# Kernel optimization log

Hardware: AMD Instinct MI355X
Metric: run time of the kernel (lower is better)

The kernel has to match this reference:

```python
import jax, jax.numpy as jnp
import numpy as np


def setup_inputs() -> dict:
    key = jax.random.key(0)
    x = jax.random.normal(key, (128, 256, 32, 32), dtype=jnp.float32)
    return {"x": x, "iter_num": 5}


def reference(x, iter_num):
    # x: (B, C, H, W)
    B, C, H, W = x.shape
    N = H * W
    xr = x.reshape(B, C, N)
    # Covariance pooling: X @ I_hat @ X^T == (1/N) * Xc @ Xc^T  (I_hat = I/N - J/N^2)
    xc = xr - xr.mean(axis=2, keepdims=True)
    cov = jnp.einsum('bcn,bdn->bcd', xc, xc) / N  # (B, C, C)

    # Newton-Schulz iterative matrix square root
    I = jnp.eye(C, dtype=x.dtype)
    I3 = 3.0 * I
    trace = jnp.trace(cov, axis1=1, axis2=2)[:, None, None]  # norm_A = tr(cov)
    A = cov / trace
    ZY = 0.5 * (I3 - A)
    Y = A @ ZY
    Z = ZY
    for _ in range(1, iter_num - 1):
        ZY = 0.5 * (I3 - Z @ Y)
        Y = Y @ ZY
        Z = ZY @ Z
    YZY = 0.5 * (Y @ (I3 - Z @ Y))
    sqrtm = YZY * jnp.sqrt(trace)  # (B, C, C)

    # Upper-triangular vectorization (row-major, including diagonal)
    r, c = np.triu_indices(C)
    idx = jnp.asarray(r * C + c)
    return sqrtm.reshape(B, C * C)[:, idx]  # (B, C*(C+1)//2)
```

## Files before the change

kernel.cpp:

```cpp
#include <hip/hip_runtime.h>
#include <hip/hip_fp16.h>


typedef _Float16 half8 __attribute__((ext_vector_type(8)));
typedef _Float16 half4 __attribute__((ext_vector_type(4)));
typedef float f32x4 __attribute__((ext_vector_type(4)));

#define OUTPB 32896

__device__ __forceinline__ void gl_lds16(const void* g, void* l) {
  __builtin_amdgcn_global_load_lds(
      (const __attribute__((address_space(1))) void*)g,
      (__attribute__((address_space(3))) void*)l, 16, 0, 0);
}

#define VMB(N) asm volatile("s_waitcnt vmcnt(" #N ")\n\ts_barrier" ::: "memory")
#define LKB()  asm volatile("s_waitcnt lgkmcnt(0)\n\ts_barrier" ::: "memory")

__device__ __forceinline__ void tile_pq(int t, int& p, int& q) {
  p = (t > 3) + (t > 6) + (t > 8);
  int base = p * 4 - (p * (p - 1)) / 2;
  q = p + (t - base);
}

__device__ __forceinline__ void mfma_buf(const _Float16* lA, const _Float16* lB,
                                         f32x4 (&acc)[2][2], int wr, int wc,
                                         int lr, int lk) {
#pragma unroll
  for (int ks = 0; ks < 4; ++ks) {
    half8 af[2], bf[2];
#pragma unroll
    for (int m = 0; m < 2; ++m) {
      int row = wr * 32 + m * 16 + lr;
      int c = (ks * 4 + lk) ^ (row & 7);
      af[m] = *(const half8*)&lA[row * 128 + c * 8];
    }
#pragma unroll
    for (int n = 0; n < 2; ++n) {
      int row = wc * 32 + n * 16 + lr;
      int c = (ks * 4 + lk) ^ (row & 7);
      bf[n] = *(const half8*)&lB[row * 128 + c * 8];
    }
    __builtin_amdgcn_s_setprio(1);
#pragma unroll
    for (int m = 0; m < 2; ++m)
#pragma unroll
      for (int n = 0; n < 2; ++n)
        acc[m][n] = __builtin_amdgcn_mfma_f32_16x16x32_f16(af[m], bf[n], acc[m][n], 0, 0, 0);
    __builtin_amdgcn_s_setprio(0);
  }
}

template <typename F>
__device__ __forceinline__ void store_sym(F f, _Float16* D, size_t boff, int p, int q,
    bool mirror, _Float16* ldsT, f32x4 (&acc)[2][2],
    int wr, int wc, int lr, int lk, int tid) {
#pragma unroll
  for (int m = 0; m < 2; ++m)
#pragma unroll
    for (int n = 0; n < 2; ++n) {
      int il0 = wr * 32 + m * 16 + lk * 4;
      int jl = wc * 32 + n * 16 + lr;
      half4 v4;
#pragma unroll
      for (int r = 0; r < 4; ++r) {
        _Float16 v = f(acc[m][n][r], p * 64 + il0 + r, q * 64 + jl);
        v4[r] = v;
        if (mirror) ldsT[(il0 + r) * 64 + (jl ^ (((il0 + r) & 7) << 3))] = v;
      }
      *(half4*)&D[boff + (size_t)(q * 64 + jl) * 256 + p * 64 + il0] = v4;
    }
  if (mirror) {
    __syncthreads();
#pragma unroll
    for (int pp = 0; pp < 2; ++pp) {
      int u = pp * 256 + tid;
      int im = u >> 3, cu = u & 7;
      half8 v8 = *(const half8*)&ldsT[im * 64 + ((cu ^ (im & 7)) << 3)];
      *(half8*)&D[boff + (size_t)(p * 64 + im) * 256 + q * 64 + cu * 8] = v8;
    }
  }
}

__global__ __launch_bounds__(256, 2) void k_cov(const float* __restrict__ x,
                                                _Float16* __restrict__ covh,
                                                float* __restrict__ trPart) {
  __shared__ _Float16 lds[32768];
  __shared__ float smA[64], smB[64], sred[4];

  const int lin = blockIdx.x + 10 * blockIdx.y;
  const int cid = (lin & 7) * 160 + (lin >> 3);
  const int b = cid / 10, t = cid - 10 * b;
  int p, q; tile_pq(t, p, q);
  const bool diag = (p == q);
  const int tid = threadIdx.x, w = tid >> 6, lane = tid & 63;
  const int wr = w >> 1, wc = w & 1, lr = lane & 15, lk = lane >> 4;

  const float* Ab = x + ((size_t)b * 256 + p * 64) * 1024;
  const float* Bb = x + ((size_t)b * 256 + q * 64) * 1024;

  float4 la[4][2], lb[4][2];
  float rsA[4] = {0.f, 0.f, 0.f, 0.f}, rsB[4] = {0.f, 0.f, 0.f, 0.f};
  f32x4 acc[2][2] = {};

  auto LOAD = [&](int kk) {
#pragma unroll
    for (int it = 0; it < 4; ++it) {
      int row = it * 16 + (tid >> 4);
      int kc = (tid & 15) ^ (row & 7);
      const float4* pa = (const float4*)(Ab + (size_t)row * 1024 + kk * 128 + kc * 8);
      la[it][0] = pa[0]; la[it][1] = pa[1];
      if (!diag) {
        const float4* pb = (const float4*)(Bb + (size_t)row * 1024 + kk * 128 + kc * 8);
        lb[it][0] = pb[0]; lb[it][1] = pb[1];
      }
    }
  };
  auto WRITE = [&](int buf) {
#pragma unroll
    for (int it = 0; it < 4; ++it) {
      int slot = it * 256 + tid;
      float4 a0 = la[it][0], a1 = la[it][1];
      rsA[it] += a0.x + a0.y + a0.z + a0.w + a1.x + a1.y + a1.z + a1.w;
      half8 h;
      h[0] = (_Float16)a0.x; h[1] = (_Float16)a0.y; h[2] = (_Float16)a0.z; h[3] = (_Float16)a0.w;
      h[4] = (_Float16)a1.x; h[5] = (_Float16)a1.y; h[6] = (_Float16)a1.z; h[7] = (_Float16)a1.w;
      *(half8*)&lds[buf * 8192 + slot * 8] = h;
      if (!diag) {
        float4 b0 = lb[it][0], b1 = lb[it][1];
        rsB[it] += b0.x + b0.y + b0.z + b0.w + b1.x + b1.y + b1.z + b1.w;
        half8 g;
        g[0] = (_Float16)b0.x; g[1] = (_Float16)b0.y; g[2] = (_Float16)b0.z; g[3] = (_Float16)b0.w;
        g[4] = (_Float16)b1.x; g[5] = (_Float16)b1.y; g[6] = (_Float16)b1.z; g[7] = (_Float16)b1.w;
        *(half8*)&lds[16384 + buf * 8192 + slot * 8] = g;
      }
    }
  };

  LOAD(0); WRITE(0); LOAD(1);
  __syncthreads();
#pragma unroll 1
  for (int kk = 0; kk < 8; ++kk) {
    int cur = kk & 1;
    mfma_buf(&lds[cur * 8192], diag ? &lds[cur * 8192] : &lds[16384 + cur * 8192],
             acc, wr, wc, lr, lk);
    if (kk < 7) {
      WRITE(cur ^ 1);
      if (kk < 6) LOAD(kk + 2);
    }
    __syncthreads();
  }

#pragma unroll
  for (int it = 0; it < 4; ++it) {
    int row = it * 16 + (tid >> 4);
    float sA = rsA[it];
    sA += __shfl_xor(sA, 1); sA += __shfl_xor(sA, 2);
    sA += __shfl_xor(sA, 4); sA += __shfl_xor(sA, 8);
    if ((lane & 15) == 0) smA[row] = sA * (1.f / 1024.f);
    if (!diag) {
      float sB = rsB[it];
      sB += __shfl_xor(sB, 1); sB += __shfl_xor(sB, 2);
      sB += __shfl_xor(sB, 4); sB += __shfl_xor(sB, 8);
      if ((lane & 15) == 0) smB[row] = sB * (1.f / 1024.f);
    }
  }
  __syncthreads();

  if (diag) {
    float tp = 0.f;
#pragma unroll
    for (int m = 0; m < 2; ++m)
#pragma unroll
      for (int n = 0; n < 2; ++n)
#pragma unroll
        for (int r = 0; r < 4; ++r) {
          int il = wr * 32 + m * 16 + lk * 4 + r, jl = wc * 32 + n * 16 + lr;
          if (il == jl) tp += acc[m][n][r] * (1.f / 1024.f) - smA[il] * smA[il];
        }
#pragma unroll
    for (int o = 32; o; o >>= 1) tp += __shfl_down(tp, o);
    if (lane == 0) sred[w] = tp;
    __syncthreads();
    if (tid == 0) trPart[b * 4 + p] = sred[0] + sred[1] + sred[2] + sred[3];
  }

  const float* smBp = diag ? smA : smB;
  store_sym([&](float a, int i, int j) {
              return (_Float16)(a * (1.f / 1024.f) - smA[i & 63] * smBp[j & 63]);
            }, covh, (size_t)b * 65536, p, q, !diag, lds, acc, wr, wc, lr, lk, tid);
}

enum { EPI_S2 = 0, EPI_ZY = 1, EPI_YZ = 2, EPI_OUT = 3 };

struct GP {
  const _Float16 *A0, *B0, *A1, *B1;
  _Float16 *D0, *D1;
  const _Float16* covh;
  const float* trP;
  float* outF;
};

template <int EPI>
__global__ __launch_bounds__(256, 2) void k_gemm(GP g) {
  __shared__ _Float16 lds[32768];

  const int lin = blockIdx.x + 10 * blockIdx.y;
  const int cid = (lin & 7) * 160 + (lin >> 3);
  const int b = cid / 10, t = cid - 10 * b;
  int p, q; tile_pq(t, p, q);
  const bool diag = (p == q);
  const bool share = diag && (EPI == EPI_S2);
  const int tid = threadIdx.x, w = tid >> 6, lane = tid & 63;
  const int wr = w >> 1, wc = w & 1, lr = lane & 15, lk = lane >> 4;

  const _Float16* Ag = g.A0;
  const _Float16* Bg = g.B0;
  _Float16* Dg = g.D0;
  if constexpr (EPI == EPI_YZ) {
    if (blockIdx.z) { Ag = g.A1; Bg = g.B1; Dg = g.D1; }
  }
  const size_t boff = (size_t)b * 65536;
  const _Float16* Ap = Ag + boff + (size_t)p * 64 * 256;
  const _Float16* Bp = Bg + boff + (size_t)q * 64 * 256;

  f32x4 acc[2][2] = {};

  auto stage1 = [&](const _Float16* M, int kk, int dstElem) {
#pragma unroll
    for (int it = 0; it < 4; ++it) {
      int row = it * 16 + (tid >> 4);
      int kc = (tid & 15) ^ (row & 7);
      gl_lds16(M + (size_t)row * 256 + kk * 128 + kc * 8,
               &lds[dstElem + (it * 256 + w * 64) * 8]);
    }
  };

  if (share) {
    stage1(Ap, 0, 0); stage1(Ap, 1, 8192);
    VMB(4);
    mfma_buf(&lds[0], &lds[0], acc, wr, wc, lr, lk);
    VMB(0);
    mfma_buf(&lds[8192], &lds[8192], acc, wr, wc, lr, lk);
  } else {
    stage1(Ap, 0, 0); stage1(Bp, 0, 16384);
    stage1(Ap, 1, 8192); stage1(Bp, 1, 24576);
    VMB(8);
    mfma_buf(&lds[0], &lds[16384], acc, wr, wc, lr, lk);
    VMB(0);
    mfma_buf(&lds[8192], &lds[24576], acc, wr, wc, lr, lk);
  }
  LKB();

  if constexpr (EPI == EPI_ZY) {
    store_sym([&](float a, int i, int j) {
                return (_Float16)((i == j ? 1.5f : 0.f) - 0.5f * a);
              }, g.D0, boff, p, q, !diag, lds, acc, wr, wc, lr, lk, tid);
  } else if constexpr (EPI == EPI_YZ) {
    store_sym([&](float a, int i, int j) { return (_Float16)a; },
              Dg, boff, p, q, !diag, lds, acc, wr, wc, lr, lk, tid);
  } else if constexpr (EPI == EPI_S2) {
    float tv = g.trP[b * 4] + g.trP[b * 4 + 1] + g.trP[b * 4 + 2] + g.trP[b * 4 + 3];
    float it1 = 1.f / tv;
    _Float16* TY = lds;
    _Float16* TZ = lds + 4096;
#pragma unroll
    for (int m = 0; m < 2; ++m)
#pragma unroll
      for (int n = 0; n < 2; ++n) {
        int il0 = wr * 32 + m * 16 + lk * 4;
        int jl = wc * 32 + n * 16 + lr;
        half4 c4 = *(const half4*)&g.covh[boff + (size_t)(q * 64 + jl) * 256 + p * 64 + il0];
        half4 y4, z4;
#pragma unroll
        for (int r = 0; r < 4; ++r) {
          int i = p * 64 + il0 + r, j = q * 64 + jl;
          float c = (float)c4[r];
          y4[r] = (_Float16)(1.5f * c * it1 - 0.5f * acc[m][n][r] * it1 * it1);
          z4[r] = (_Float16)((i == j ? 1.5f : 0.f) - 0.5f * c * it1);
          if (!diag) {
            int sp = (il0 + r) * 64 + (jl ^ (((il0 + r) & 7) << 3));
            TY[sp] = y4[r]; TZ[sp] = z4[r];
          }
        }
        *(half4*)&g.D0[boff + (size_t)(q * 64 + jl) * 256 + p * 64 + il0] = y4;
        *(half4*)&g.D1[boff + (size_t)(q * 64 + jl) * 256 + p * 64 + il0] = z4;
      }
    if (!diag) {
      __syncthreads();
#pragma unroll
      for (int pp = 0; pp < 2; ++pp) {
        int u = pp * 256 + tid;
        int im = u >> 3, cu = u & 7;
        half8 vy = *(const half8*)&TY[im * 64 + ((cu ^ (im & 7)) << 3)];
        half8 vz = *(const half8*)&TZ[im * 64 + ((cu ^ (im & 7)) << 3)];
        *(half8*)&g.D0[boff + (size_t)(p * 64 + im) * 256 + q * 64 + cu * 8] = vy;
        *(half8*)&g.D1[boff + (size_t)(p * 64 + im) * 256 + q * 64 + cu * 8] = vz;
      }
    }
  } else {
    float tv = g.trP[b * 4] + g.trP[b * 4 + 1] + g.trP[b * 4 + 2] + g.trP[b * 4 + 3];
    float st = sqrtf(tv);
#pragma unroll
    for (int m = 0; m < 2; ++m)
#pragma unroll
      for (int n = 0; n < 2; ++n)
#pragma unroll
        for (int r = 0; r < 4; ++r) {
          int i = p * 64 + wr * 32 + m * 16 + lk * 4 + r;
          int j = q * 64 + wc * 32 + n * 16 + lr;
          if (i <= j) {
            int idx = j + i * 256 - (i * (i + 1)) / 2;
            g.outF[(size_t)b * OUTPB + idx] = acc[m][n][r] * st;
          }
        }
  }
}

extern "C" void kernel_launch(void* const* d_in, const int* in_sizes, int n_in,
                              void* d_out, int out_size, void* d_ws, size_t ws_size,
                              hipStream_t stream) {
  const float* x = (const float*)d_in[0];
  float* outF = (float*)d_out;

  char* ws = (char*)d_ws;
  size_t off = 0;
  auto alloc = [&](size_t bytes) -> void* {
    void* pt = ws + off;
    off = (off + bytes + 255) & ~(size_t)255;
    return pt;
  };
  const size_t MATB = (size_t)128 * 65536 * sizeof(_Float16);
  _Float16* covh = (_Float16*)alloc(MATB);
  _Float16* Y0 = (_Float16*)alloc(MATB);
  _Float16* Z0 = (_Float16*)alloc(MATB);
  _Float16* Y1 = (_Float16*)alloc(MATB);
  _Float16* Z1 = (_Float16*)alloc(MATB);
  float* trP = (float*)alloc(512 * sizeof(float));

  dim3 g10(10, 128), g10z(10, 128, 2);

  k_cov<<<g10, 256, 0, stream>>>(x, covh, trP);

  {
    GP a{};
    a.A0 = covh; a.B0 = covh; a.D0 = Y0; a.D1 = Z0;
    a.covh = covh; a.trP = trP;
    k_gemm<EPI_S2><<<g10, 256, 0, stream>>>(a);
  }

  _Float16 *Yc = Y0, *Zc = Z0, *Yn = Y1, *Zn = Z1;
  for (int itn = 0; itn < 3; ++itn) {
    GP a{};
    a.A0 = Zc; a.B0 = Yc; a.D0 = covh;
    k_gemm<EPI_ZY><<<g10, 256, 0, stream>>>(a);
    GP r{};
    r.A0 = Yc; r.B0 = covh; r.D0 = Yn;
    r.A1 = covh; r.B1 = Zc; r.D1 = Zn;
    k_gemm<EPI_YZ><<<g10z, 256, 0, stream>>>(r);
    _Float16* t0 = Yc; Yc = Yn; Yn = t0;
    _Float16* t1 = Zc; Zc = Zn; Zn = t1;
  }
  {
    GP a{};
    a.A0 = Zc; a.B0 = Yc; a.D0 = covh;
    k_gemm<EPI_ZY><<<g10, 256, 0, stream>>>(a);
    GP o{};
    o.A0 = Yc; o.B0 = covh; o.trP = trP; o.outF = outF;
    k_gemm<EPI_OUT><<<g10, 256, 0, stream>>>(o);
  }
}
```

Baseline: 179.6 us.

## Restructure cov and GEMM kernels with async LDS staging and fused Y/Z update

The covariance kernel now stages fp32 input straight into LDS with global_load_lds and converts to fp16 while reading fragments. Row sums for mean-centering come from extra MFMAs against a ones vector instead of scalar adds and shuffles. The GEMM kernels switch to 64-wide K steps with double buffering, smaller LDS, and higher occupancy. A new k_yzm kernel computes Y@W and Z@W together so the shared W operand is loaded once and the z-dimension launch goes away. The cost is twice the fp32 LDS footprint in k_cov, extra MFMAs for the row sums, and more barriers per tile.

After: 169.8 us. 5.5% less time.

```diff
diff --git a/kernel.cpp b/kernel.cpp
--- a/kernel.cpp
+++ b/kernel.cpp
@@ -23,23 +23,30 @@
   q = p + (t - base);
 }
 
-__device__ __forceinline__ void mfma_buf(const _Float16* lA, const _Float16* lB,
-                                         f32x4 (&acc)[2][2], int wr, int wc,
-                                         int lr, int lk) {
-#pragma unroll
-  for (int ks = 0; ks < 4; ++ks) {
+__device__ __forceinline__ half8 cvt8(float4 a, float4 b) {
+  half8 h;
+  h[0] = (_Float16)a.x; h[1] = (_Float16)a.y; h[2] = (_Float16)a.z; h[3] = (_Float16)a.w;
+  h[4] = (_Float16)b.x; h[5] = (_Float16)b.y; h[6] = (_Float16)b.z; h[7] = (_Float16)b.w;
+  return h;
+}
+
+__device__ __forceinline__ void mfma64(const _Float16* lA, const _Float16* lB,
+                                       f32x4 (&acc)[2][2], int wr, int wc,
+                                       int lr, int lk) {
+#pragma unroll
+  for (int ks = 0; ks < 2; ++ks) {
     half8 af[2], bf[2];
 #pragma unroll
     for (int m = 0; m < 2; ++m) {
       int row = wr * 32 + m * 16 + lr;
-      int c = (ks * 4 + lk) ^ (row & 7);
-      af[m] = *(const half8*)&lA[row * 128 + c * 8];
+      int kc = (ks * 4 + lk) ^ (row & 7);
+      af[m] = *(const half8*)&lA[row * 64 + kc * 8];
     }
 #pragma unroll
     for (int n = 0; n < 2; ++n) {
       int row = wc * 32 + n * 16 + lr;
-      int c = (ks * 4 + lk) ^ (row & 7);
-      bf[n] = *(const half8*)&lB[row * 128 + c * 8];
+      int kc = (ks * 4 + lk) ^ (row & 7);
+      bf[n] = *(const half8*)&lB[row * 64 + kc * 8];
     }
     __builtin_amdgcn_s_setprio(1);
 #pragma unroll
@@ -85,8 +92,8 @@
 __global__ __launch_bounds__(256, 2) void k_cov(const float* __restrict__ x,
                                                 _Float16* __restrict__ covh,
                                                 float* __restrict__ trPart) {
-  __shared__ _Float16 lds[32768];
-  __shared__ float smA[64], smB[64], sred[4];
+  __shared__ float lds_f[16384];
+  __shared__ float sred[4];
 
   const int lin = blockIdx.x + 10 * blockIdx.y;
   const int cid = (lin & 7) * 160 + (lin >> 3);
@@ -99,74 +106,76 @@
   const float* Ab = x + ((size_t)b * 256 + p * 64) * 1024;
   const float* Bb = x + ((size_t)b * 256 + q * 64) * 1024;
 
-  float4 la[4][2], lb[4][2];
-  float rsA[4] = {0.f, 0.f, 0.f, 0.f}, rsB[4] = {0.f, 0.f, 0.f, 0.f};
   f32x4 acc[2][2] = {};
-
-  auto LOAD = [&](int kk) {
-#pragma unroll
-    for (int it = 0; it < 4; ++it) {
-      int row = it * 16 + (tid >> 4);
-      int kc = (tid & 15) ^ (row & 7);
-      const float4* pa = (const float4*)(Ab + (size_t)row * 1024 + kk * 128 + kc * 8);
-      la[it][0] = pa[0]; la[it][1] = pa[1];
-      if (!diag) {
-        const float4* pb = (const float4*)(Bb + (size_t)row * 1024 + kk * 128 + kc * 8);
-        lb[it][0] = pb[0]; lb[it][1] = pb[1];
-      }
+  f32x4 rsA[2] = {}, rsB[2] = {};
+  half8 ones;
+#pragma unroll
+  for (int i = 0; i < 8; ++i) ones[i] = (_Float16)1.0f;
+
+  auto stageF = [&](const float* panel, int buf, int baseF, int kk) {
+#pragma unroll
+    for (int i = 0; i < 4; ++i) {
+      int s = (w * 4 + i) * 64 + lane;
+      int row = s >> 4, cst = s & 15;
+      int kc = cst ^ (row & 15);
+      gl_lds16(panel + (size_t)row * 1024 + kk * 64 + kc * 4,
+               &lds_f[baseF + buf * 4096 + (w * 4 + i) * 256]);
     }
   };
-  auto WRITE = [&](int buf) {
-#pragma unroll
-    for (int it = 0; it < 4; ++it) {
-      int slot = it * 256 + tid;
-      float4 a0 = la[it][0], a1 = la[it][1];
-      rsA[it] += a0.x + a0.y + a0.z + a0.w + a1.x + a1.y + a1.z + a1.w;
-      half8 h;
-      h[0] = (_Float16)a0.x; h[1] = (_Float16)a0.y; h[2] = (_Float16)a0.z; h[3] = (_Float16)a0.w;
-      h[4] = (_Float16)a1.x; h[5] = (_Float16)a1.y; h[6] = (_Float16)a1.z; h[7] = (_Float16)a1.w;
-      *(half8*)&lds[buf * 8192 + slot * 8] = h;
-      if (!diag) {
-        float4 b0 = lb[it][0], b1 = lb[it][1];
-        rsB[it] += b0.x + b0.y + b0.z + b0.w + b1.x + b1.y + b1.z + b1.w;
-        half8 g;
-        g[0] = (_Float16)b0.x; g[1] = (_Float16)b0.y; g[2] = (_Float16)b0.z; g[3] = (_Float16)b0.w;
-        g[4] = (_Float16)b1.x; g[5] = (_Float16)b1.y; g[6] = (_Float16)b1.z; g[7] = (_Float16)b1.w;
-        *(half8*)&lds[16384 + buf * 8192 + slot * 8] = g;
-      }
+
+  auto step = [&](const float* lA, const float* lB) {
+#pragma unroll
+    for (int ks = 0; ks < 2; ++ks) {
+      half8 af[2], bf[2];
+#pragma unroll
+      for (int m = 0; m < 2; ++m) {
+        int row = wr * 32 + m * 16 + lr;
+        int msk = row & 15, c0 = ks * 8 + lk * 2;
+        float4 f0 = *(const float4*)&lA[row * 64 + (c0 ^ msk) * 4];
+        float4 f1 = *(const float4*)&lA[row * 64 + ((c0 + 1) ^ msk) * 4];
+        af[m] = cvt8(f0, f1);
+      }
+#pragma unroll
+      for (int n = 0; n < 2; ++n) {
+        int row = wc * 32 + n * 16 + lr;
+        int msk = row & 15, c0 = ks * 8 + lk * 2;
+        float4 f0 = *(const float4*)&lB[row * 64 + (c0 ^ msk) * 4];
+        float4 f1 = *(const float4*)&lB[row * 64 + ((c0 + 1) ^ msk) * 4];
+        bf[n] = cvt8(f0, f1);
+      }
+      __builtin_amdgcn_s_setprio(1);
+#pragma unroll
+      for (int m = 0; m < 2; ++m)
+        rsA[m] = __builtin_amdgcn_mfma_f32_16x16x32_f16(af[m], ones, rsA[m], 0, 0, 0);
+#pragma unroll
+      for (int n = 0; n < 2; ++n)
+        rsB[n] = __builtin_amdgcn_mfma_f32_16x16x32_f16(ones, bf[n], rsB[n], 0, 0, 0);
+#pragma unroll
+      for (int m = 0; m < 2; ++m)
+#pragma unroll
+        for (int n = 0; n < 2; ++n)
+          acc[m][n] = __builtin_amdgcn_mfma_f32_16x16x32_f16(af[m], bf[n], acc[m][n], 0, 0, 0);
+      __builtin_amdgcn_s_setprio(0);
     }
   };
 
-  LOAD(0); WRITE(0); LOAD(1);
-  __syncthreads();
+  stageF(Ab, 0, 0, 0);
+  if (!diag) stageF(Bb, 0, 8192, 0);
 #pragma unroll 1
-  for (int kk = 0; kk < 8; ++kk) {
+  for (int kk = 0; kk < 16; ++kk) {
     int cur = kk & 1;
-    mfma_buf(&lds[cur * 8192], diag ? &lds[cur * 8192] : &lds[16384 + cur * 8192],
-             acc, wr, wc, lr, lk);
-    if (kk < 7) {
-      WRITE(cur ^ 1);
-      if (kk < 6) LOAD(kk + 2);
-    }
-    __syncthreads();
-  }
-
-#pragma unroll
-  for (int it = 0; it < 4; ++it) {
-    int row = it * 16 + (tid >> 4);
-    float sA = rsA[it];
-    sA += __shfl_xor(sA, 1); sA += __shfl_xor(sA, 2);
-    sA += __shfl_xor(sA, 4); sA += __shfl_xor(sA, 8);
-    if ((lane & 15) == 0) smA[row] = sA * (1.f / 1024.f);
-    if (!diag) {
-      float sB = rsB[it];
-      sB += __shfl_xor(sB, 1); sB += __shfl_xor(sB, 2);
-      sB += __shfl_xor(sB, 4); sB += __shfl_xor(sB, 8);
-      if ((lane & 15) == 0) smB[row] = sB * (1.f / 1024.f);
-    }
-  }
-  __syncthreads();
-
+    if (kk < 15) {
+      stageF(Ab, cur ^ 1, 0, kk + 1);
+      if (!diag) stageF(Bb, cur ^ 1, 8192, kk + 1);
+      if (diag) { VMB(4); } else { VMB(8); }
+    } else {
+      VMB(0);
+    }
+    step(&lds_f[cur * 4096], diag ? &lds_f[cur * 4096] : &lds_f[8192 + cur * 4096]);
+    LKB();
+  }
+
+  const float inv = 1.f / 1024.f;
   if (diag) {
     float tp = 0.f;
 #pragma unroll
@@ -176,7 +185,7 @@
 #pragma unroll
         for (int r = 0; r < 4; ++r) {
           int il = wr * 32 + m * 16 + lk * 4 + r, jl = wc * 32 + n * 16 + lr;
-          if (il == jl) tp += acc[m][n][r] * (1.f / 1024.f) - smA[il] * smA[il];
+          if (il == jl) tp += (acc[m][n][r] - rsA[m][r] * rsB[n][0] * inv) * inv;
         }
 #pragma unroll
     for (int o = 32; o; o >>= 1) tp += __shfl_down(tp, o);
@@ -185,16 +194,39 @@
     if (tid == 0) trPart[b * 4 + p] = sred[0] + sred[1] + sred[2] + sred[3];
   }
 
-  const float* smBp = diag ? smA : smB;
-  store_sym([&](float a, int i, int j) {
-              return (_Float16)(a * (1.f / 1024.f) - smA[i & 63] * smBp[j & 63]);
-            }, covh, (size_t)b * 65536, p, q, !diag, lds, acc, wr, wc, lr, lk, tid);
-}
-
-enum { EPI_S2 = 0, EPI_ZY = 1, EPI_YZ = 2, EPI_OUT = 3 };
+  _Float16* ldsh = (_Float16*)lds_f;
+  const size_t boff = (size_t)b * 65536;
+#pragma unroll
+  for (int m = 0; m < 2; ++m)
+#pragma unroll
+    for (int n = 0; n < 2; ++n) {
+      int il0 = wr * 32 + m * 16 + lk * 4;
+      int jl = wc * 32 + n * 16 + lr;
+      half4 v4;
+#pragma unroll
+      for (int r = 0; r < 4; ++r) {
+        float cv = (acc[m][n][r] - rsA[m][r] * rsB[n][0] * inv) * inv;
+        v4[r] = (_Float16)cv;
+        if (!diag) ldsh[(il0 + r) * 64 + (jl ^ (((il0 + r) & 7) << 3))] = v4[r];
+      }
+      *(half4*)&covh[boff + (size_t)(q * 64 + jl) * 256 + p * 64 + il0] = v4;
+    }
+  if (!diag) {
+    __syncthreads();
+#pragma unroll
+    for (int pp = 0; pp < 2; ++pp) {
+      int u = pp * 256 + tid;
+      int im = u >> 3, cu = u & 7;
+      half8 v8 = *(const half8*)&ldsh[im * 64 + ((cu ^ (im & 7)) << 3)];
+      *(half8*)&covh[boff + (size_t)(p * 64 + im) * 256 + q * 64 + cu * 8] = v8;
+    }
+  }
+}
+
+enum { EPI_S2 = 0, EPI_ZY = 1, EPI_OUT = 2 };
 
 struct GP {
-  const _Float16 *A0, *B0, *A1, *B1;
+  const _Float16 *A0, *B0;
   _Float16 *D0, *D1;
   const _Float16* covh;
   const float* trP;
@@ -202,63 +234,56 @@
 };
 
 template <int EPI>
-__global__ __launch_bounds__(256, 2) void k_gemm(GP g) {
-  __shared__ _Float16 lds[32768];
+__global__ __launch_bounds__(256, 4) void k_gemm(GP g) {
+  __shared__ _Float16 lds[(EPI == EPI_S2) ? 8192 : 16384];
 
   const int lin = blockIdx.x + 10 * blockIdx.y;
   const int cid = (lin & 7) * 160 + (lin >> 3);
   const int b = cid / 10, t = cid - 10 * b;
   int p, q; tile_pq(t, p, q);
   const bool diag = (p == q);
-  const bool share = diag && (EPI == EPI_S2);
+  constexpr bool share = (EPI == EPI_S2);
   const int tid = threadIdx.x, w = tid >> 6, lane = tid & 63;
   const int wr = w >> 1, wc = w & 1, lr = lane & 15, lk = lane >> 4;
 
-  const _Float16* Ag = g.A0;
-  const _Float16* Bg = g.B0;
-  _Float16* Dg = g.D0;
-  if constexpr (EPI == EPI_YZ) {
-    if (blockIdx.z) { Ag = g.A1; Bg = g.B1; Dg = g.D1; }
-  }
   const size_t boff = (size_t)b * 65536;
-  const _Float16* Ap = Ag + boff + (size_t)p * 64 * 256;
-  const _Float16* Bp = Bg + boff + (size_t)q * 64 * 256;
+  const _Float16* Ap = g.A0 + boff + (size_t)p * 64 * 256;
+  const _Float16* Bp = (share ? g.A0 : g.B0) + boff + (size_t)q * 64 * 256;
 
   f32x4 acc[2][2] = {};
 
-  auto stage1 = [&](const _Float16* M, int kk, int dstElem) {
-#pragma unroll
-    for (int it = 0; it < 4; ++it) {
-      int row = it * 16 + (tid >> 4);
-      int kc = (tid & 15) ^ (row & 7);
-      gl_lds16(M + (size_t)row * 256 + kk * 128 + kc * 8,
-               &lds[dstElem + (it * 256 + w * 64) * 8]);
+  auto stageH = [&](const _Float16* panel, int buf, int base, int kk) {
+#pragma unroll
+    for (int i = 0; i < 2; ++i) {
+      int s = (w * 2 + i) * 64 + lane;
+      int row = s >> 3, cst = s & 7;
+      int kc = cst ^ (row & 7);
+      gl_lds16(panel + (size_t)row * 256 + kk * 64 + kc * 8,
+               &lds[base + buf * 4096 + (w * 2 + i) * 512]);
     }
   };
 
-  if (share) {
-    stage1(Ap, 0, 0); stage1(Ap, 1, 8192);
-    VMB(4);
-    mfma_buf(&lds[0], &lds[0], acc, wr, wc, lr, lk);
-    VMB(0);
-    mfma_buf(&lds[8192], &lds[8192], acc, wr, wc, lr, lk);
-  } else {
-    stage1(Ap, 0, 0); stage1(Bp, 0, 16384);
-    stage1(Ap, 1, 8192); stage1(Bp, 1, 24576);
-    VMB(8);
-    mfma_buf(&lds[0], &lds[16384], acc, wr, wc, lr, lk);
-    VMB(0);
-    mfma_buf(&lds[8192], &lds[24576], acc, wr, wc, lr, lk);
-  }
-  LKB();
+  stageH(Ap, 0, 0, 0);
+  if (!share) stageH(Bp, 0, 8192, 0);
+#pragma unroll 1
+  for (int kk = 0; kk < 4; ++kk) {
+    int cur = kk & 1;
+    if (kk < 3) {
+      stageH(Ap, cur ^ 1, 0, kk + 1);
+      if (!share) stageH(Bp, cur ^ 1, 8192, kk + 1);
+      if (share) { VMB(2); } else { VMB(4); }
+    } else {
+      VMB(0);
+    }
+    mfma64(&lds[cur * 4096], share ? &lds[cur * 4096] : &lds[8192 + cur * 4096],
+           acc, wr, wc, lr, lk);
+    LKB();
+  }
 
   if constexpr (EPI == EPI_ZY) {
     store_sym([&](float a, int i, int j) {
                 return (_Float16)((i == j ? 1.5f : 0.f) - 0.5f * a);
               }, g.D0, boff, p, q, !diag, lds, acc, wr, wc, lr, lk, tid);
-  } else if constexpr (EPI == EPI_YZ) {
-    store_sym([&](float a, int i, int j) { return (_Float16)a; },
-              Dg, boff, p, q, !diag, lds, acc, wr, wc, lr, lk, tid);
   } else if constexpr (EPI == EPI_S2) {
     float tv = g.trP[b * 4] + g.trP[b * 4 + 1] + g.trP[b * 4 + 2] + g.trP[b * 4 + 3];
     float it1 = 1.f / tv;
@@ -314,6 +339,120 @@
             g.outF[(size_t)b * OUTPB + idx] = acc[m][n][r] * st;
           }
         }
+  }
+}
+
+struct YZP {
+  const _Float16 *Y, *Z, *W;
+  _Float16 *Yn, *Zn;
+};
+
+__global__ __launch_bounds__(256, 3) void k_yzm(YZP g) {
+  __shared__ _Float16 lds[24576];
+
+  const int lin = blockIdx.x + 10 * blockIdx.y;
+  const int cid = (lin & 7) * 160 + (lin >> 3);
+  const int b = cid / 10, t = cid - 10 * b;
+  int p, q; tile_pq(t, p, q);
+  const bool diag = (p == q);
+  const int tid = threadIdx.x, w = tid >> 6, lane = tid & 63;
+  const int wr = w >> 1, wc = w & 1, lr = lane & 15, lk = lane >> 4;
+
+  const size_t boff = (size_t)b * 65536;
+  const _Float16* Yp = g.Y + boff + (size_t)p * 64 * 256;
+  const _Float16* Zp = g.Z + boff + (size_t)p * 64 * 256;
+  const _Float16* Wp = g.W + boff + (size_t)q * 64 * 256;
+
+  f32x4 accY[2][2] = {}, accZ[2][2] = {};
+
+  auto stageH = [&](const _Float16* panel, int buf, int base, int kk) {
+#pragma unroll
+    for (int i = 0; i < 2; ++i) {
+      int s = (w * 2 + i) * 64 + lane;
+      int row = s >> 3, cst = s & 7;
+      int kc = cst ^ (row & 7);
+      gl_lds16(panel + (size_t)row * 256 + kk * 64 + kc * 8,
+               &lds[base + buf * 4096 + (w * 2 + i) * 512]);
+    }
+  };
+
+  auto step = [&](const _Float16* lY, const _Float16* lZ, const _Float16* lW) {
+#pragma unroll
+    for (int ks = 0; ks < 2; ++ks) {
+      half8 yf[2], zf[2], wf[2];
+#pragma unroll
+      for (int m = 0; m < 2; ++m) {
+        int row = wr * 32 + m * 16 + lr;
+        int kc = (ks * 4 + lk) ^ (row & 7);
+        yf[m] = *(const half8*)&lY[row * 64 + kc * 8];
+        zf[m] = *(const half8*)&lZ[row * 64 + kc * 8];
+      }
+#pragma unroll
+      for (int n = 0; n < 2; ++n) {
+        int row = wc * 32 + n * 16 + lr;
+        int kc = (ks * 4 + lk) ^ (row & 7);
+        wf[n] = *(const half8*)&lW[row * 64 + kc * 8];
+      }
+      __builtin_amdgcn_s_setprio(1);
+#pragma unroll
+      for (int m = 0; m < 2; ++m)
+#pragma unroll
+        for (int n = 0; n < 2; ++n) {
+          accY[m][n] = __builtin_amdgcn_mfma_f32_16x16x32_f16(yf[m], wf[n], accY[m][n], 0, 0, 0);
+          accZ[m][n] = __builtin_amdgcn_mfma_f32_16x16x32_f16(zf[m], wf[n], accZ[m][n], 0, 0, 0);
+        }
+      __builtin_amdgcn_s_setprio(0);
+    }
+  };
+
+  stageH(Yp, 0, 0, 0); stageH(Zp, 0, 8192, 0); stageH(Wp, 0, 16384, 0);
+#pragma unroll 1
+  for (int kk = 0; kk < 4; ++kk) {
+    int cur = kk & 1;
+    if (kk < 3) {
+      stageH(Yp, cur ^ 1, 0, kk + 1);
+      stageH(Zp, cur ^ 1, 8192, kk + 1);
+      stageH(Wp, cur ^ 1, 16384, kk + 1);
+      VMB(6);
+    } else {
+      VMB(0);
+    }
+    step(&lds[cur * 4096], &lds[8192 + cur * 4096], &lds[16384 + cur * 4096]);
+    LKB();
+  }
+
+  _Float16* TY = lds;
+  _Float16* TZ = lds + 4096;
+#pragma unroll
+  for (int m = 0; m < 2; ++m)
+#pragma unroll
+    for (int n = 0; n < 2; ++n) {
+      int il0 = wr * 32 + m * 16 + lk * 4;
+      int jl = wc * 32 + n * 16 + lr;
+      half4 y4, z4;
+#pragma unroll
+      for (int r = 0; r < 4; ++r) {
+        y4[r] = (_Float16)accY[m][n][r];
+        z4[r] = (_Float16)accZ[m][n][r];
+        if (!diag) {
+          int sp = (il0 + r) * 64 + (jl ^ (((il0 + r) & 7) << 3));
+          TY[sp] = y4[r]; TZ[sp] = z4[r];
+        }
+      }
+      *(half4*)&g.Yn[boff + (size_t)(q * 64 + jl) * 256 + p * 64 + il0] = y4;
+      *(half4*)&g.Zn[boff + (size_t)(q * 64 + jl) * 256 + p * 64 + il0] = z4;
+    }
+  if (!diag) {
+    __syncthreads();
+#pragma unroll
+    for (int pp = 0; pp < 2; ++pp) {
+      int u = pp * 256 + tid;
+      int im = u >> 3, cu = u & 7;
+      half8 vy = *(const half8*)&TY[im * 64 + ((cu ^ (im & 7)) << 3)];
+      half8 vz = *(const half8*)&TZ[im * 64 + ((cu ^ (im & 7)) << 3)];
+      *(half8*)&g.Yn[boff + (size_t)(p * 64 + im) * 256 + q * 64 + cu * 8] = vy;
+      *(half8*)&g.Zn[boff + (size_t)(p * 64 + im) * 256 + q * 64 + cu * 8] = vz;
+    }
   }
 }
 
@@ -338,13 +477,13 @@
   _Float16* Z1 = (_Float16*)alloc(MATB);
   float* trP = (float*)alloc(512 * sizeof(float));
 
-  dim3 g10(10, 128), g10z(10, 128, 2);
+  dim3 g10(10, 128);
 
   k_cov<<<g10, 256, 0, stream>>>(x, covh, trP);
 
   {
     GP a{};
-    a.A0 = covh; a.B0 = covh; a.D0 = Y0; a.D1 = Z0;
+    a.A0 = covh; a.D0 = Y0; a.D1 = Z0;
     a.covh = covh; a.trP = trP;
     k_gemm<EPI_S2><<<g10, 256, 0, stream>>>(a);
   }
@@ -354,10 +493,9 @@
     GP a{};
     a.A0 = Zc; a.B0 = Yc; a.D0 = covh;
     k_gemm<EPI_ZY><<<g10, 256, 0, stream>>>(a);
-    GP r{};
-    r.A0 = Yc; r.B0 = covh; r.D0 = Yn;
-    r.A1 = covh; r.B1 = Zc; r.D1 = Zn;
-    k_gemm<EPI_YZ><<<g10z, 256, 0, stream>>>(r);
+    YZP r{};
+    r.Y = Yc; r.Z = Zc; r.W = covh; r.Yn = Yn; r.Zn = Zn;
+    k_yzm<<<g10, 256, 0, stream>>>(r);
     _Float16* t0 = Yc; Yc = Yn; Yn = t0;
     _Float16* t1 = Zc; Zc = Zn; Zn = t1;
   }
```
